# Performance work log

Hardware: AMD Instinct MI355X
Metric: run time of the kernel (lower is better)

Reference implementation:

```python
import jax, jax.numpy as jnp
import numpy as np
from jax import lax

BIG = jnp.float32(1e10)  # initial 'infinite' min-distance


def farthest_point_sampling(points, nsamples):
    """Exact iterative FPS. points: (B, P, 3) -> indices (B, nsamples) int32.

    The KD-tree partitioning in QuickFPS is an acceleration structure; the
    reference math is the canonical running-min-distance / argmax FPS.
    """
    B, P, _ = points.shape

    def step(carry, _):
        min_d, last_idx = carry
        # (B, 1, 3) coordinates of the most recently selected point
        last_pt = jnp.take_along_axis(points, last_idx[:, None, None], axis=1)
        d = jnp.sum((points - last_pt) ** 2, axis=-1)  # (B, P)
        min_d = jnp.minimum(min_d, d)
        nxt = jnp.argmax(min_d, axis=-1).astype(jnp.int32)  # (B,)
        return (min_d, nxt), nxt

    init_idx = jnp.zeros((B,), jnp.int32)  # CUDA FPS starts from point 0
    init_d = jnp.full((B, P), BIG, dtype=points.dtype)
    (_, _), rest = lax.scan(step, (init_d, init_idx), None, length=nsamples - 1)
    # rest: (nsamples-1, B) -> (B, nsamples)
    indices = jnp.concatenate([init_idx[None, :], rest], axis=0).T
    return indices


def setup_inputs() -> dict:
    key = jax.random.key(0)
    points = jax.random.normal(key, (32, 65536, 3), dtype=jnp.float32)
    return {"points": points}


def reference(points):
    nsamples = 1024
    indices = farthest_point_sampling(points, nsamples)  # (B, nsamples)
    # gather_points: (B, nsamples, 3)
    sampled_points = jnp.take_along_axis(points, indices[:, :, None], axis=1)
    return indices, sampled_points
```

## Files before the change

### kernel.cpp

```cpp
#include <hip/hip_runtime.h>

#define NB 32
#define NP 65536
#define NS 1024
#define NT 1024
#define BPB 8
#define CHUNK (NP / BPB)
#define PPT2 (CHUNK / NT)

typedef unsigned long long u64;
typedef unsigned int u32;
typedef int int4v __attribute__((ext_vector_type(4)));

__global__ __launch_bounds__(NT) void fps_v6(const float* __restrict__ pts,
                                             float* __restrict__ out,
                                             u32* __restrict__ slots) {
#pragma clang fp contract(off)
    const int bid = blockIdx.x;
    const int b = bid >> 3;
    const int j = bid & 7;
    const int t = threadIdx.x;
    const int base = j * CHUNK;
    const float* __restrict__ pb = pts + (size_t)b * NP * 3;
    float* __restrict__ out_idx = out + (size_t)b * NS;
    float* __restrict__ out_pts = out + (size_t)NB * NS + (size_t)b * NS * 3;
    u32* __restrict__ slot_b = slots + (size_t)b * NS * BPB * 8;

    __shared__ float4 P4[CHUNK];
    __shared__ u64 cand[NT / 64];
    __shared__ int sel_hist[NS];
    __shared__ float qsh[3];

    {
        const float4* __restrict__ src4 = (const float4*)(pb + (size_t)base * 3);
#pragma unroll
        for (int k2 = 0; k2 < CHUNK / 4 / NT; ++k2) {
            const int g = t + k2 * NT;
            float4 A = src4[g * 3 + 0];
            float4 B = src4[g * 3 + 1];
            float4 C = src4[g * 3 + 2];
            P4[g * 4 + 0] = make_float4(A.x, A.y, A.z, 0.f);
            P4[g * 4 + 1] = make_float4(A.w, B.x, B.y, 0.f);
            P4[g * 4 + 2] = make_float4(B.z, B.w, C.x, 0.f);
            P4[g * 4 + 3] = make_float4(C.y, C.z, C.w, 0.f);
        }
    }

    float md[PPT2];
#pragma unroll
    for (int i = 0; i < PPT2; ++i) md[i] = 1e10f;

    if (t == 0) {
        sel_hist[0] = 0;
        if (j == 0) out_idx[0] = 0.0f;
        qsh[0] = pb[0]; qsh[1] = pb[1]; qsh[2] = pb[2];
    }
    __syncthreads();

    float qx = qsh[0], qy = qsh[1], qz = qsh[2];

    const int wave = t >> 6;
    const int lane = t & 63;

    for (int s = 1; s < NS; ++s) {
        float bestv = -1.0f;
        int besti = 0;
#pragma unroll
        for (int i = 0; i < PPT2; ++i) {
            const int li = t + i * NT;
            float4 p = P4[li];
            float dx = p.x - qx;
            float dy = p.y - qy;
            float dz = p.z - qz;
            float d = (dx * dx + dy * dy) + dz * dz;
            float nmd = fminf(md[i], d);
            md[i] = nmd;
            if (nmd > bestv) { bestv = nmd; besti = li; }
        }
        u64 pk = ((u64)__float_as_uint(bestv) << 32) |
                 (u64)(0xFFFFFFFFu - (u32)(base + besti));
#pragma unroll
        for (int m = 32; m >= 1; m >>= 1) {
            u64 o = __shfl_xor(pk, m, 64);
            pk = (o > pk) ? o : pk;
        }
        if (lane == 0) cand[wave] = pk;
        __syncthreads();
        if (wave == 0) {
            u64 c = (lane < 16) ? cand[lane] : 0ull;
#pragma unroll
            for (int m = 8; m >= 1; m >>= 1) {
                u64 o = __shfl_xor(c, m, 64);
                c = (o > c) ? o : c;
            }
            if (lane == 0) {
                const int gwin = (int)(0xFFFFFFFFu - (u32)(c & 0xFFFFFFFFull));
                const int lwin = gwin - base;
                float4 pw = P4[lwin];
                int4v h0, h1;
                h0.x = (int)(u32)(c & 0xFFFFFFFFull);
                h0.y = (int)(u32)(c >> 32);
                h0.z = __float_as_int(pw.x);
                h0.w = __float_as_int(pw.y);
                h1.x = h0.x;
                h1.y = h0.y;
                h1.z = __float_as_int(pw.z);
                h1.w = 0;
                u32* sp = slot_b + ((size_t)s * BPB + j) * 8;
                asm volatile(
                    "global_store_dwordx4 %0, %2, off sc0 sc1\n\t"
                    "global_store_dwordx4 %1, %3, off sc0 sc1"
                    :: "v"(sp), "v"(sp + 4), "v"(h0), "v"(h1) : "memory");
            }
            u64 k = 0;
            float wx = 0.f, wy = 0.f, wz = 0.f;
            if (lane < BPB) {
                const u32* pp = slot_b + ((size_t)s * BPB + lane) * 8;
                int4v a, bb;
                for (;;) {
                    asm volatile(
                        "global_load_dwordx4 %0, %2, off sc0 sc1\n\t"
                        "global_load_dwordx4 %1, %3, off sc0 sc1\n\t"
                        "s_waitcnt vmcnt(0)"
                        : "=&v"(a), "=&v"(bb)
                        : "v"(pp), "v"(pp + 4) : "memory");
                    if (a.x != 0 && a.x == bb.x && a.y == bb.y) break;
                    __builtin_amdgcn_s_sleep(1);
                }
                k = ((u64)(u32)a.y << 32) | (u32)a.x;
                wx = __int_as_float(a.z);
                wy = __int_as_float(a.w);
                wz = __int_as_float(bb.z);
            }
#pragma unroll
            for (int m = 4; m >= 1; m >>= 1) {
                u64 o = __shfl_xor(k, m, 64);
                k = (o > k) ? o : k;
            }
            const int g = (int)(0xFFFFFFFFu - (u32)(k & 0xFFFFFFFFull));
            const int jw = (g >> 13) & 7;
            float sx = __shfl(wx, jw, 64);
            float sy = __shfl(wy, jw, 64);
            float sz = __shfl(wz, jw, 64);
            if (lane == 0) {
                sel_hist[s] = g;
                qsh[0] = sx; qsh[1] = sy; qsh[2] = sz;
                if (j == 0) out_idx[s] = (float)g;
            }
        }
        __syncthreads();
        qx = qsh[0]; qy = qsh[1]; qz = qsh[2];
    }

    if (j == 0) {
        const int gi = sel_hist[t];
        const float* __restrict__ p = pb + (size_t)gi * 3;
        out_pts[(size_t)t * 3 + 0] = p[0];
        out_pts[(size_t)t * 3 + 1] = p[1];
        out_pts[(size_t)t * 3 + 2] = p[2];
    }
}

__global__ __launch_bounds__(NT) void fps_slots(const float* __restrict__ pts,
                                                float* __restrict__ out,
                                                u64* __restrict__ slots) {
#pragma clang fp contract(off)
    const int bid = blockIdx.x;
    const int b = bid >> 3;
    const int j = bid & 7;
    const int t = threadIdx.x;
    const int base = j * CHUNK;
    const float* __restrict__ pb = pts + (size_t)b * NP * 3;
    float* __restrict__ out_idx = out + (size_t)b * NS;
    float* __restrict__ out_pts = out + (size_t)NB * NS + (size_t)b * NS * 3;
    u64* __restrict__ slot_b = slots + (size_t)b * NS * BPB;

    __shared__ float P[CHUNK * 3];
    __shared__ u64 cand[NT / 64];
    __shared__ int sel_hist[NS];
    __shared__ float qsh[3];

    {
        const float4* __restrict__ src4 = (const float4*)(pb + (size_t)base * 3);
        float4* dst4 = (float4*)P;
#pragma unroll
        for (int k = 0; k < (CHUNK * 3 / 4) / NT; ++k) dst4[t + k * NT] = src4[t + k * NT];
    }
    float md[PPT2];
#pragma unroll
    for (int i = 0; i < PPT2; ++i) md[i] = 1e10f;
    if (t == 0) {
        sel_hist[0] = 0;
        if (j == 0) out_idx[0] = 0.0f;
        qsh[0] = pb[0]; qsh[1] = pb[1]; qsh[2] = pb[2];
    }
    __syncthreads();
    float qx = qsh[0], qy = qsh[1], qz = qsh[2];
    const int wave = t >> 6;
    const int lane = t & 63;
    for (int s = 1; s < NS; ++s) {
        float bestv = -1.0f;
        int besti = 0;
#pragma unroll
        for (int i = 0; i < PPT2; ++i) {
            const int li = t + i * NT;
            const float* __restrict__ p = P + li * 3;
            float dx = p[0] - qx, dy = p[1] - qy, dz = p[2] - qz;
            float d = (dx * dx + dy * dy) + dz * dz;
            float nmd = fminf(md[i], d);
            md[i] = nmd;
            if (nmd > bestv) { bestv = nmd; besti = li; }
        }
        u64 pk = ((u64)__float_as_uint(bestv) << 32) |
                 (u64)(0xFFFFFFFFu - (u32)(base + besti));
#pragma unroll
        for (int m = 32; m >= 1; m >>= 1) {
            u64 o = __shfl_xor(pk, m, 64);
            pk = (o > pk) ? o : pk;
        }
        if (lane == 0) cand[wave] = pk;
        __syncthreads();
        if (wave == 0) {
            u64 c = (lane < 16) ? cand[lane] : 0ull;
#pragma unroll
            for (int m = 8; m >= 1; m >>= 1) {
                u64 o = __shfl_xor(c, m, 64);
                c = (o > c) ? o : c;
            }
            if (lane == 0) {
                __hip_atomic_store(&slot_b[(size_t)s * BPB + j], c,
                                   __ATOMIC_RELAXED, __HIP_MEMORY_SCOPE_AGENT);
            }
            u64 x = 0;
            if (lane < BPB) {
                const u64* sp = &slot_b[(size_t)s * BPB + lane];
                while ((x = __hip_atomic_load(sp, __ATOMIC_RELAXED,
                                              __HIP_MEMORY_SCOPE_AGENT)) == 0ull) {
                    __builtin_amdgcn_s_sleep(1);
                }
            }
#pragma unroll
            for (int m = 4; m >= 1; m >>= 1) {
                u64 o = __shfl_xor(x, m, 64);
                x = (o > x) ? o : x;
            }
            if (lane == 0) {
                int w = (int)(0xFFFFFFFFu - (u32)(x & 0xFFFFFFFFull));
                sel_hist[s] = w;
                const float* __restrict__ q = pb + (size_t)w * 3;
                qsh[0] = q[0]; qsh[1] = q[1]; qsh[2] = q[2];
                if (j == 0) out_idx[s] = (float)w;
            }
        }
        __syncthreads();
        qx = qsh[0]; qy = qsh[1]; qz = qsh[2];
    }
    if (j == 0) {
        const int gi = sel_hist[t];
        const float* __restrict__ p = pb + (size_t)gi * 3;
        out_pts[(size_t)t * 3 + 0] = p[0];
        out_pts[(size_t)t * 3 + 1] = p[1];
        out_pts[(size_t)t * 3 + 2] = p[2];
    }
}

extern "C" void kernel_launch(void* const* d_in, const int* in_sizes, int n_in,
                              void* d_out, int out_size, void* d_ws, size_t ws_size,
                              hipStream_t stream) {
    const float* pts = (const float*)d_in[0];
    float* out = (float*)d_out;
    (void)in_sizes; (void)n_in; (void)out_size;

    const size_t v6_bytes = (size_t)NB * NS * BPB * 32;
    const size_t slot_bytes = (size_t)NB * NS * BPB * sizeof(u64);
    if (ws_size >= v6_bytes) {
        u32* slots = (u32*)d_ws;
        hipMemsetAsync(d_ws, 0, v6_bytes, stream);
        void* args[] = {(void*)&pts, (void*)&out, (void*)&slots};
        hipLaunchCooperativeKernel((const void*)fps_v6, dim3(NB * BPB), dim3(NT),
                                   args, 0, stream);
    } else {
        u64* slots = (u64*)d_ws;
        hipMemsetAsync(d_ws, 0, slot_bytes, stream);
        void* args[] = {(void*)&pts, (void*)&out, (void*)&slots};
        hipLaunchCooperativeKernel((const void*)fps_slots, dim3(NB * BPB), dim3(NT),
                                   args, 0, stream);
    }
}
```

Measured before the change: 2.558 ms.

## Keep points in registers, skip own slot poll, drop spin sleep in FPS

```diff
diff --git a/kernel.cpp b/kernel.cpp
--- a/kernel.cpp
+++ b/kernel.cpp
@@ -12,7 +12,7 @@
 typedef unsigned int u32;
 typedef int int4v __attribute__((ext_vector_type(4)));
 
-__global__ __launch_bounds__(NT) void fps_v6(const float* __restrict__ pts,
+__global__ __launch_bounds__(NT) void fps_v7(const float* __restrict__ pts,
                                              float* __restrict__ out,
                                              u32* __restrict__ slots) {
 #pragma clang fp contract(off)
@@ -26,29 +26,17 @@
     float* __restrict__ out_pts = out + (size_t)NB * NS + (size_t)b * NS * 3;
     u32* __restrict__ slot_b = slots + (size_t)b * NS * BPB * 8;
 
-    __shared__ float4 P4[CHUNK];
+    __shared__ float P[CHUNK * 3];
     __shared__ u64 cand[NT / 64];
     __shared__ int sel_hist[NS];
     __shared__ float qsh[3];
 
     {
         const float4* __restrict__ src4 = (const float4*)(pb + (size_t)base * 3);
-#pragma unroll
-        for (int k2 = 0; k2 < CHUNK / 4 / NT; ++k2) {
-            const int g = t + k2 * NT;
-            float4 A = src4[g * 3 + 0];
-            float4 B = src4[g * 3 + 1];
-            float4 C = src4[g * 3 + 2];
-            P4[g * 4 + 0] = make_float4(A.x, A.y, A.z, 0.f);
-            P4[g * 4 + 1] = make_float4(A.w, B.x, B.y, 0.f);
-            P4[g * 4 + 2] = make_float4(B.z, B.w, C.x, 0.f);
-            P4[g * 4 + 3] = make_float4(C.y, C.z, C.w, 0.f);
-        }
-    }
-
-    float md[PPT2];
-#pragma unroll
-    for (int i = 0; i < PPT2; ++i) md[i] = 1e10f;
+        float4* dst4 = (float4*)P;
+#pragma unroll
+        for (int k = 0; k < (CHUNK * 3 / 4) / NT; ++k) dst4[t + k * NT] = src4[t + k * NT];
+    }
 
     if (t == 0) {
         sel_hist[0] = 0;
@@ -57,6 +45,16 @@
     }
     __syncthreads();
 
+    float px[PPT2], py[PPT2], pz[PPT2], md[PPT2];
+#pragma unroll
+    for (int i = 0; i < PPT2; ++i) {
+        const int li = t + i * NT;
+        px[i] = P[li * 3 + 0];
+        py[i] = P[li * 3 + 1];
+        pz[i] = P[li * 3 + 2];
+        md[i] = 1e10f;
+    }
+
     float qx = qsh[0], qy = qsh[1], qz = qsh[2];
 
     const int wave = t >> 6;
@@ -67,15 +65,13 @@
         int besti = 0;
 #pragma unroll
         for (int i = 0; i < PPT2; ++i) {
-            const int li = t + i * NT;
-            float4 p = P4[li];
-            float dx = p.x - qx;
-            float dy = p.y - qy;
-            float dz = p.z - qz;
+            float dx = px[i] - qx;
+            float dy = py[i] - qy;
+            float dz = pz[i] - qz;
             float d = (dx * dx + dy * dy) + dz * dz;
             float nmd = fminf(md[i], d);
             md[i] = nmd;
-            if (nmd > bestv) { bestv = nmd; besti = li; }
+            if (nmd > bestv) { bestv = nmd; besti = t + i * NT; }
         }
         u64 pk = ((u64)__float_as_uint(bestv) << 32) |
                  (u64)(0xFFFFFFFFu - (u32)(base + besti));
@@ -87,24 +83,27 @@
         if (lane == 0) cand[wave] = pk;
         __syncthreads();
         if (wave == 0) {
-            u64 c = (lane < 16) ? cand[lane] : 0ull;
+            u64 c = cand[lane & 15];
 #pragma unroll
             for (int m = 8; m >= 1; m >>= 1) {
                 u64 o = __shfl_xor(c, m, 64);
                 c = (o > c) ? o : c;
             }
+            const int g0 = (int)(0xFFFFFFFFu - (u32)(c & 0xFFFFFFFFull));
+            float wx0 = 0.f, wy0 = 0.f, wz0 = 0.f;
             if (lane == 0) {
-                const int gwin = (int)(0xFFFFFFFFu - (u32)(c & 0xFFFFFFFFull));
-                const int lwin = gwin - base;
-                float4 pw = P4[lwin];
+                const int lw = g0 - base;
+                wx0 = P[lw * 3 + 0];
+                wy0 = P[lw * 3 + 1];
+                wz0 = P[lw * 3 + 2];
                 int4v h0, h1;
                 h0.x = (int)(u32)(c & 0xFFFFFFFFull);
                 h0.y = (int)(u32)(c >> 32);
-                h0.z = __float_as_int(pw.x);
-                h0.w = __float_as_int(pw.y);
+                h0.z = __float_as_int(wx0);
+                h0.w = __float_as_int(wy0);
                 h1.x = h0.x;
                 h1.y = h0.y;
-                h1.z = __float_as_int(pw.z);
+                h1.z = __float_as_int(wz0);
                 h1.w = 0;
                 u32* sp = slot_b + ((size_t)s * BPB + j) * 8;
                 asm volatile(
@@ -112,40 +111,43 @@
                     "global_store_dwordx4 %1, %3, off sc0 sc1"
                     :: "v"(sp), "v"(sp + 4), "v"(h0), "v"(h1) : "memory");
             }
-            u64 k = 0;
-            float wx = 0.f, wy = 0.f, wz = 0.f;
             if (lane < BPB) {
-                const u32* pp = slot_b + ((size_t)s * BPB + lane) * 8;
-                int4v a, bb;
-                for (;;) {
-                    asm volatile(
-                        "global_load_dwordx4 %0, %2, off sc0 sc1\n\t"
-                        "global_load_dwordx4 %1, %3, off sc0 sc1\n\t"
-                        "s_waitcnt vmcnt(0)"
-                        : "=&v"(a), "=&v"(bb)
-                        : "v"(pp), "v"(pp + 4) : "memory");
-                    if (a.x != 0 && a.x == bb.x && a.y == bb.y) break;
-                    __builtin_amdgcn_s_sleep(1);
-                }
-                k = ((u64)(u32)a.y << 32) | (u32)a.x;
-                wx = __int_as_float(a.z);
-                wy = __int_as_float(a.w);
-                wz = __int_as_float(bb.z);
-            }
-#pragma unroll
-            for (int m = 4; m >= 1; m >>= 1) {
-                u64 o = __shfl_xor(k, m, 64);
-                k = (o > k) ? o : k;
-            }
-            const int g = (int)(0xFFFFFFFFu - (u32)(k & 0xFFFFFFFFull));
-            const int jw = (g >> 13) & 7;
-            float sx = __shfl(wx, jw, 64);
-            float sy = __shfl(wy, jw, 64);
-            float sz = __shfl(wz, jw, 64);
-            if (lane == 0) {
-                sel_hist[s] = g;
-                qsh[0] = sx; qsh[1] = sy; qsh[2] = sz;
-                if (j == 0) out_idx[s] = (float)g;
+                u64 k = 0;
+                float wx = 0.f, wy = 0.f, wz = 0.f;
+                if (lane != j) {
+                    const u32* pp = slot_b + ((size_t)s * BPB + lane) * 8;
+                    int4v a, bb;
+                    for (;;) {
+                        asm volatile(
+                            "global_load_dwordx4 %0, %2, off sc0 sc1\n\t"
+                            "global_load_dwordx4 %1, %3, off sc0 sc1\n\t"
+                            "s_waitcnt vmcnt(0)"
+                            : "=&v"(a), "=&v"(bb)
+                            : "v"(pp), "v"(pp + 4) : "memory");
+                        if (a.x != 0 && a.x == bb.x && a.y == bb.y) break;
+                    }
+                    k = ((u64)(u32)a.y << 32) | (u32)a.x;
+                    wx = __int_as_float(a.z);
+                    wy = __int_as_float(a.w);
+                    wz = __int_as_float(bb.z);
+                }
+                u64 mx = (c > k) ? c : k;
+#pragma unroll
+                for (int m = 4; m >= 1; m >>= 1) {
+                    u64 o = __shfl_xor(mx, m, 64);
+                    mx = (o > mx) ? o : mx;
+                }
+                const int g = (int)(0xFFFFFFFFu - (u32)(mx & 0xFFFFFFFFull));
+                const int jw = (g >> 13) & 7;
+                float sx = __shfl(wx, jw, 64);
+                float sy = __shfl(wy, jw, 64);
+                float sz = __shfl(wz, jw, 64);
+                if (lane == 0) {
+                    sel_hist[s] = g;
+                    if (jw == j) { qsh[0] = wx0; qsh[1] = wy0; qsh[2] = wz0; }
+                    else         { qsh[0] = sx;  qsh[1] = sy;  qsh[2] = sz;  }
+                    if (j == 0) out_idx[s] = (float)g;
+                }
             }
         }
         __syncthreads();
@@ -271,13 +273,13 @@
     float* out = (float*)d_out;
     (void)in_sizes; (void)n_in; (void)out_size;
 
-    const size_t v6_bytes = (size_t)NB * NS * BPB * 32;
+    const size_t v7_bytes = (size_t)NB * NS * BPB * 32;
     const size_t slot_bytes = (size_t)NB * NS * BPB * sizeof(u64);
-    if (ws_size >= v6_bytes) {
+    if (ws_size >= v7_bytes) {
         u32* slots = (u32*)d_ws;
-        hipMemsetAsync(d_ws, 0, v6_bytes, stream);
+        hipMemsetAsync(d_ws, 0, v7_bytes, stream);
         void* args[] = {(void*)&pts, (void*)&out, (void*)&slots};
-        hipLaunchCooperativeKernel((const void*)fps_v6, dim3(NB * BPB), dim3(NT),
+        hipLaunchCooperativeKernel((const void*)fps_v7, dim3(NB * BPB), dim3(NT),
                                    args, 0, stream);
     } else {
         u64* slots = (u64*)d_ws;
```

After: 2.222 ms. 1.15x faster.
